# Performance work log

Measured on AMD Instinct MI355X. Metric: run time of the kernel, lower is better.

Reference implementation:

```python
import jax, jax.numpy as jnp
import numpy as np

B, S, D, H, N = 2, 2048, 768, 12, 128  # batch, seq_len, d_model, n_heads, num_segments
EPS_LN = 1e-5


def _layer_norm(x, g, b):
    m = x.mean(-1, keepdims=True)
    v = ((x - m) ** 2).mean(-1, keepdims=True)
    return (x - m) / jnp.sqrt(v + EPS_LN) * g + b


def _mha(q, k, v, Wqkv, bqkv, Wo, bo, n_heads):
    """torch.nn.MultiheadAttention (batch_first), returns (out, head-averaged attn)."""
    d = q.shape[-1]
    dh = d // n_heads
    Wq, Wk, Wv = jnp.split(Wqkv, 3, axis=0)
    bq, bk, bv = jnp.split(bqkv, 3)
    qh = (q @ Wq.T + bq).reshape(q.shape[0], q.shape[1], n_heads, dh)
    kh = (k @ Wk.T + bk).reshape(k.shape[0], k.shape[1], n_heads, dh)
    vh = (v @ Wv.T + bv).reshape(v.shape[0], v.shape[1], n_heads, dh)
    scores = jnp.einsum('bqhd,bkhd->bhqk', qh, kh) / jnp.sqrt(jnp.asarray(dh, q.dtype))
    attn = jax.nn.softmax(scores, axis=-1)                      # [B,H,Sq,Sk]
    out = jnp.einsum('bhqk,bkhd->bqhd', attn, vh).reshape(q.shape[0], q.shape[1], d)
    return out @ Wo.T + bo, attn.mean(axis=1)                   # attn avg over heads


def _aggregate(x, w, seg):  # per-batch: weighted mean of tokens into N segments
    num = jax.ops.segment_sum(w[:, None] * x, seg, num_segments=N)
    den = jax.ops.segment_sum(w, seg, num_segments=N)
    return num / (den[:, None] + 1e-8)


def setup_inputs() -> dict:
    key = jax.random.key(0)
    ks = jax.random.split(key, 16)
    s = 0.02
    inp = {
        'hidden_states': jax.random.normal(ks[0], (B, S, D), jnp.float32),
        'token_to_segment': jnp.sort(jax.random.randint(ks[1], (B, S), 0, N), axis=-1),
        # token_attention (shared for node-level self-attn in the adjacency=None branch)
        'Wqkv_t': jax.random.normal(ks[2], (3 * D, D), jnp.float32) * s,
        'bqkv_t': jnp.zeros((3 * D,), jnp.float32),
        'Wo_t': jax.random.normal(ks[3], (D, D), jnp.float32) * s,
        'bo_t': jnp.zeros((D,), jnp.float32),
        # cross_attention
        'Wqkv_c': jax.random.normal(ks[4], (3 * D, D), jnp.float32) * s,
        'bqkv_c': jnp.zeros((3 * D,), jnp.float32),
        'Wo_c': jax.random.normal(ks[5], (D, D), jnp.float32) * s,
        'bo_c': jnp.zeros((D,), jnp.float32),
        # layer norms
        'g_tok': jnp.ones((D,), jnp.float32),
        'b_tok': jnp.zeros((D,), jnp.float32),
        'g_node': jnp.ones((D,), jnp.float32),
        'b_node': jnp.zeros((D,), jnp.float32),
        # output projection
        'W_out': jax.random.normal(ks[6], (D, D), jnp.float32) * s,
        'b_out': jnp.zeros((D,), jnp.float32),
    }
    return inp


def reference(hidden_states, token_to_segment, Wqkv_t, bqkv_t, Wo_t, bo_t,
              Wqkv_c, bqkv_c, Wo_c, bo_c, g_tok, b_tok, g_node, b_node,
              W_out, b_out):
    hs = hidden_states
    # token-level self-attention + residual norm
    tok_attn_out, tok_attn = _mha(hs, hs, hs, Wqkv_t, bqkv_t, Wo_t, bo_t, H)
    token_output = _layer_norm(hs + tok_attn_out, g_tok, b_tok)
    # token -> node attention-weighted scatter aggregation
    w = tok_attn.mean(axis=1)  # [B,S] attention received per token
    node_emb = jax.vmap(_aggregate)(token_output, w, token_to_segment)  # [B,N,D]
    # node-level self-attention (reuses token_attention weights; adjacency=None path)
    node_out, node_attn = _mha(node_emb, node_emb, node_emb, Wqkv_t, bqkv_t, Wo_t, bo_t, H)
    node_emb = _layer_norm(node_emb + node_out, g_node, b_node)
    # cross-attention: tokens attend to nodes
    cross_out, cross_w = _mha(token_output, node_emb, node_emb, Wqkv_c, bqkv_c, Wo_c, bo_c, H)
    token_output = token_output + cross_out
    # node -> token gather + additive combine
    gathered = jnp.take_along_axis(node_emb, token_to_segment[:, :, None], axis=1)  # [B,S,D]
    enhanced = token_output + gathered
    output = enhanced @ W_out.T + b_out
    return output, node_emb, tok_attn, node_attn, cross_w
```

## Files before the change

### kernel.cpp

```cpp
#include <hip/hip_runtime.h>
#include <cstdint>

#define B_ 2
#define S_ 2048
#define D_ 768
#define H_ 12
#define DH_ 64
#define N_ 128

typedef unsigned short u16;
typedef unsigned int u32;
typedef unsigned long long u64;
typedef __attribute__((ext_vector_type(8))) short short8;
typedef __attribute__((ext_vector_type(4))) float f32x4;

#define MFMA16(a, b, c) __builtin_amdgcn_mfma_f32_16x16x32_bf16(a, b, c, 0, 0, 0)

__device__ inline u16 f2bf(float f) {
  union { float f; u32 u; } v; v.f = f;
  u32 r = v.u + 0x7FFFu + ((v.u >> 16) & 1u);
  return (u16)(r >> 16);
}
__device__ inline u32 pk2(float a, float b) {
  return (u32)f2bf(a) | ((u32)f2bf(b) << 16);
}
__device__ inline float bf2f(u16 h) {
  union { u32 u; float f; } v; v.u = ((u32)h) << 16;
  return v.f;
}
__device__ inline float wredmax(float v) {
  #pragma unroll
  for (int o = 32; o > 0; o >>= 1) v = fmaxf(v, __shfl_down(v, o));
  return v;
}
__device__ inline float wredsum(float v) {
  #pragma unroll
  for (int o = 32; o > 0; o >>= 1) v += __shfl_down(v, o);
  return v;
}
__device__ inline void async_lds16(const u16* g, u16* l) {
  __builtin_amdgcn_global_load_lds((const __attribute__((address_space(1))) void*)g,
                                   (__attribute__((address_space(3))) void*)l, 16, 0, 0);
}

__global__ void conv_bf16(const float* __restrict__ in, u16* __restrict__ outp, int n8) {
  int i = blockIdx.x * 256 + threadIdx.x;
  if (i >= n8) return;
  const float4* p = (const float4*)(in + (size_t)i * 8);
  float4 a = p[0], b = p[1];
  uint4 u;
  u.x = pk2(a.x, a.y); u.y = pk2(a.z, a.w); u.z = pk2(b.x, b.y); u.w = pk2(b.z, b.w);
  *(uint4*)(outp + (size_t)i * 8) = u;
}

template <int OUT_BF16>
__global__ __launch_bounds__(256) void gemm_bf16(
    const u16* __restrict__ A, int lda,
    const u16* __restrict__ W, int ldb,
    const float* __restrict__ bias,
    void* __restrict__ Cout, int ldc, int K) {
  __shared__ u16 As[128 * 32];
  __shared__ u16 Ws[128 * 32];
  const int tid = threadIdx.x;
  const int m0 = blockIdx.y * 128, n0 = blockIdx.x * 128;
  const int w = tid >> 6, lane = tid & 63;
  const int msub = (w & 1) * 64, nsub = (w >> 1) * 64;
  const int lrow = lane & 15, quad = lane >> 4;
  const int e0 = tid * 8;
  const int r0 = e0 >> 5, c0 = e0 & 31;
  const int e1 = e0 + 2048;
  const int r1 = e1 >> 5, c1 = e1 & 31;
  const u16* Ag0 = A + (size_t)(m0 + r0) * lda + c0;
  const u16* Ag1 = A + (size_t)(m0 + r1) * lda + c1;
  const u16* Wg0 = W + (size_t)(n0 + r0) * ldb + c0;
  const u16* Wg1 = W + (size_t)(n0 + r1) * ldb + c1;
  u16* AsB0 = As + (w << 9);
  u16* AsB1 = As + 2048 + (w << 9);
  u16* WsB0 = Ws + (w << 9);
  u16* WsB1 = Ws + 2048 + (w << 9);
  f32x4 zero = {0.f, 0.f, 0.f, 0.f};
  f32x4 acc[4][4];
  #pragma unroll
  for (int i = 0; i < 4; i++)
    #pragma unroll
    for (int j = 0; j < 4; j++) acc[i][j] = zero;
  for (int k0 = 0; k0 < K; k0 += 32) {
    __syncthreads();
    async_lds16(Ag0 + k0, AsB0);
    async_lds16(Ag1 + k0, AsB1);
    async_lds16(Wg0 + k0, WsB0);
    async_lds16(Wg1 + k0, WsB1);
    __syncthreads();
    short8 af[4], bf[4];
    #pragma unroll
    for (int i = 0; i < 4; i++)
      af[i] = *(const short8*)(As + (msub + i * 16 + lrow) * 32 + quad * 8);
    #pragma unroll
    for (int j = 0; j < 4; j++)
      bf[j] = *(const short8*)(Ws + (nsub + j * 16 + lrow) * 32 + quad * 8);
    #pragma unroll
    for (int i = 0; i < 4; i++)
      #pragma unroll
      for (int j = 0; j < 4; j++)
        acc[i][j] = MFMA16(af[i], bf[j], acc[i][j]);
  }
  #pragma unroll
  for (int i = 0; i < 4; i++) {
    #pragma unroll
    for (int j = 0; j < 4; j++) {
      int col = n0 + nsub + j * 16 + lrow;
      float bv = bias ? bias[col] : 0.f;
      #pragma unroll
      for (int r = 0; r < 4; r++) {
        int row = m0 + msub + i * 16 + quad * 4 + r;
        float val = acc[i][j][r] + bv;
        if (OUT_BF16) ((u16*)Cout)[(size_t)row * ldc + col] = f2bf(val);
        else ((float*)Cout)[(size_t)row * ldc + col] = val;
      }
    }
  }
}

__global__ __launch_bounds__(256) void transpose_v(const u16* __restrict__ qkv, u16* __restrict__ VT) {
  __shared__ u16 t[64][72];
  const int z = blockIdx.y, b = z / 12, h = z - b * 12;
  const int s0 = blockIdx.x * 64;
  const int tid = threadIdx.x;
  {
    int r = tid >> 2, dp = (tid & 3) * 16;
    const u16* src = qkv + (size_t)b * 2048 * 2304 + (size_t)(s0 + r) * 2304 + 1536 + h * 64 + dp;
    *(uint4*)&t[r][dp] = *(const uint4*)src;
    *(uint4*)&t[r][dp + 8] = *(const uint4*)(src + 8);
  }
  __syncthreads();
  int d = tid >> 2, sp = (tid & 3) * 16;
  u16 vals[16];
  #pragma unroll
  for (int i = 0; i < 16; i++) vals[i] = t[sp + i][d];
  u16* dst = VT + ((size_t)z * 64 + d) * 2048 + s0 + sp;
  *(uint4*)dst = *(uint4*)&vals[0];
  *(uint4*)(dst + 8) = *(uint4*)&vals[8];
}

__global__ __launch_bounds__(512, 2) void fused_tok_attn(
    const u16* __restrict__ qkv, const u16* __restrict__ VT,
    float* __restrict__ am, u16* __restrict__ attnout) {
  __shared__ u16 pbuf[8][16][264];
  __shared__ float lred[8][16];
  __shared__ float obuf[8][16][66];
  const int tid = threadIdx.x;
  const int w = tid >> 6, lane = tid & 63;
  const int lrow = lane & 15, quad = lane >> 4;
  const int blk = blockIdx.x;
  const int b = blk >> 7, q0 = (blk & 127) << 4;
  const u16* qp = qkv + (size_t)b * 2048 * 2304;
  const u16* kp = qp + 768;
  const int strip = w * 256;
  float* amrow = am + (size_t)b * 2048 * 2048 + (size_t)(q0 + lrow) * 2048 + strip;
  u16* ob = attnout + (size_t)b * 2048 * 768 + (size_t)q0 * 768;
  u16* pb = &pbuf[w][0][0];
  const float c12 = 1.f / 12.f;
  f32x4 zero = {0.f, 0.f, 0.f, 0.f};
  float amreg[8][8];
  #pragma unroll
  for (int c = 0; c < 8; c++)
    #pragma unroll
    for (int e = 0; e < 8; e++) amreg[c][e] = 0.f;
  for (int h = 0; h < 12; h++) {
    const u16* qh = qp + (size_t)(q0 + lrow) * 2304 + h * 64 + quad * 8;
    short8 qf0 = *(const short8*)qh;
    short8 qf1 = *(const short8*)(qh + 32);
    float lsum = 0.f;
    #pragma unroll
    for (int t = 0; t < 16; t++) {
      const u16* kh = kp + (size_t)(strip + t * 16 + lrow) * 2304 + h * 64 + quad * 8;
      short8 kf0 = *(const short8*)kh;
      short8 kf1 = *(const short8*)(kh + 32);
      f32x4 sv = zero;
      sv = MFMA16(kf0, qf0, sv);
      sv = MFMA16(kf1, qf1, sv);
      float pe0 = __expf(sv[0] * 0.125f);
      float pe1 = __expf(sv[1] * 0.125f);
      float pe2 = __expf(sv[2] * 0.125f);
      float pe3 = __expf(sv[3] * 0.125f);
      lsum += (pe0 + pe1) + (pe2 + pe3);
      u32 w0 = pk2(pe0, pe1), w1 = pk2(pe2, pe3);
      *(u64*)(pb + lrow * 264 + t * 16 + quad * 4) = (u64)w0 | ((u64)w1 << 32);
    }
    lsum += __shfl_xor(lsum, 16);
    lsum += __shfl_xor(lsum, 32);
    if (lane < 16) lred[w][lane] = lsum;
    __syncthreads();
    float invq;
    float inv4[4];
    {
      float s = 0.f;
      #pragma unroll
      for (int w2 = 0; w2 < 8; w2++) s += lred[w2][lrow];
      invq = 1.f / s;
      #pragma unroll
      for (int r = 0; r < 4; r++) {
        float sr = 0.f;
        #pragma unroll
        for (int w2 = 0; w2 < 8; w2++) sr += lred[w2][quad * 4 + r];
        inv4[r] = 1.f / sr;
      }
    }
    f32x4 oacc[4];
    #pragma unroll
    for (int j = 0; j < 4; j++) oacc[j] = zero;
    const u16* vtp = VT + (size_t)(b * 12 + h) * 64 * 2048;
    #pragma unroll
    for (int c = 0; c < 8; c++) {
      short8 pf = *(const short8*)(pb + lrow * 264 + c * 32 + quad * 8);
      short8 vf[4];
      #pragma unroll
      for (int j = 0; j < 4; j++)
        vf[j] = *(const short8*)(vtp + (size_t)(j * 16 + lrow) * 2048 + strip + c * 32 + quad * 8);
      #pragma unroll
      for (int j = 0; j < 4; j++) oacc[j] = MFMA16(pf, vf[j], oacc[j]);
      #pragma unroll
      for (int e = 0; e < 8; e++)
        amreg[c][e] += bf2f((u16)pf[e]) * invq;
    }
    asm volatile("s_waitcnt lgkmcnt(0)" ::: "memory");
    __builtin_amdgcn_sched_barrier(0);
    #pragma unroll
    for (int j = 0; j < 4; j++)
      #pragma unroll
      for (int r = 0; r < 4; r++)
        obuf[w][quad * 4 + r][j * 16 + lrow] = oacc[j][r] * inv4[r];
    __syncthreads();
    #pragma unroll
    for (int ee = 0; ee < 2; ee++) {
      int e2 = tid + ee * 512;
      int row = e2 >> 6, col = e2 & 63;
      float s = 0.f;
      #pragma unroll
      for (int w2 = 0; w2 < 8; w2++) s += obuf[w2][row][col];
      ob[(size_t)row * 768 + h * 64 + col] = f2bf(s);
    }
    __syncthreads();
  }
  #pragma unroll
  for (int c = 0; c < 8; c++) {
    float4 v0 = {amreg[c][0] * c12, amreg[c][1] * c12, amreg[c][2] * c12, amreg[c][3] * c12};
    float4 v1 = {amreg[c][4] * c12, amreg[c][5] * c12, amreg[c][6] * c12, amreg[c][7] * c12};
    *(float4*)(amrow + c * 32 + quad * 8) = v0;
    *(float4*)(amrow + c * 32 + quad * 8 + 4) = v1;
  }
}

__global__ __launch_bounds__(256) void qk_mfma(
    const u16* __restrict__ Q, int ldq, long qbs,
    const u16* __restrict__ Kp, int ldk, long kbs,
    float* __restrict__ S, long szs, int Sk, int nh, float scale) {
  __shared__ u16 Qs[128 * 72];
  __shared__ u16 Ks[128 * 72];
  const int tid = threadIdx.x;
  const int z = blockIdx.z, bb = z / nh, h = z - bb * nh;
  const u16* qp = Q + (size_t)bb * qbs + h * 64;
  const u16* kp = Kp + (size_t)bb * kbs + h * 64;
  float* sp = S + (size_t)z * szs;
  const int m0 = blockIdx.y * 128, n0 = blockIdx.x * 128;
  const int w = tid >> 6, lane = tid & 63;
  const int msub = (w & 1) * 64, nsub = (w >> 1) * 64;
  const int lrow = lane & 15, quad = lane >> 4;
  const int srow = tid >> 1, shalf = tid & 1;
  {
    const uint4* qg = (const uint4*)(qp + (size_t)(m0 + srow) * ldq + shalf * 32);
    const uint4* kg = (const uint4*)(kp + (size_t)(n0 + srow) * ldk + shalf * 32);
    uint4* qd = (uint4*)(Qs + srow * 72 + shalf * 32);
    uint4* kd = (uint4*)(Ks + srow * 72 + shalf * 32);
    #pragma unroll
    for (int u = 0; u < 4; u++) { qd[u] = qg[u]; kd[u] = kg[u]; }
  }
  __syncthreads();
  f32x4 zero = {0.f, 0.f, 0.f, 0.f};
  f32x4 acc[4][4];
  #pragma unroll
  for (int i = 0; i < 4; i++)
    #pragma unroll
    for (int j = 0; j < 4; j++) acc[i][j] = zero;
  #pragma unroll
  for (int ks = 0; ks < 2; ks++) {
    short8 af[4], bf[4];
    #pragma unroll
    for (int i = 0; i < 4; i++)
      af[i] = *(const short8*)(Qs + (msub + i * 16 + lrow) * 72 + ks * 32 + quad * 8);
    #pragma unroll
    for (int j = 0; j < 4; j++)
      bf[j] = *(const short8*)(Ks + (nsub + j * 16 + lrow) * 72 + ks * 32 + quad * 8);
    #pragma unroll
    for (int i = 0; i < 4; i++)
      #pragma unroll
      for (int j = 0; j < 4; j++)
        acc[i][j] = MFMA16(af[i], bf[j], acc[i][j]);
  }
  #pragma unroll
  for (int i = 0; i < 4; i++)
    #pragma unroll
    for (int j = 0; j < 4; j++) {
      int col = n0 + nsub + j * 16 + lrow;
      #pragma unroll
      for (int r = 0; r < 4; r++) {
        int row = m0 + msub + i * 16 + quad * 4 + r;
        sp[(size_t)row * Sk + col] = acc[i][j][r] * scale;
      }
    }
}

__global__ __launch_bounds__(128) void softmax_small(
    float* __restrict__ Sc, float* __restrict__ wout, int Sq) {
  const int q = blockIdx.x, b = blockIdx.y, tid = threadIdx.x;
  const int w = tid >> 6, lane = tid & 63;
  __shared__ float red[2];
  float am = 0.f;
  const size_t plane = (size_t)Sq * 128;
  for (int h = 0; h < 12; h++) {
    const int z = b * 12 + h;
    float* row = Sc + (size_t)z * plane + (size_t)q * 128;
    float v = row[tid];
    float m = wredmax(v);
    if (lane == 0) red[w] = m;
    __syncthreads();
    m = fmaxf(red[0], red[1]);
    float e = __expf(v - m);
    float s = wredsum(e);
    __syncthreads();
    if (lane == 0) red[w] = s;
    __syncthreads();
    float p = e / (red[0] + red[1]);
    ((u16*)(Sc + (size_t)z * plane))[(size_t)q * 256 + tid] = f2bf(p);
    am += p;
    __syncthreads();
  }
  wout[((size_t)b * Sq + q) * 128 + tid] = am * (1.f / 12.f);
}

__global__ __launch_bounds__(256) void pv_small(
    const u16* __restrict__ Pb, long pzs,
    const u16* __restrict__ KVb, int ldv, long vbs, int vhoff,
    u16* __restrict__ Outb, long obs) {
  __shared__ u16 Ps[128 * 40];
  __shared__ u16 Vs[64 * 40];
  const int tid = threadIdx.x;
  const int z = blockIdx.y, b = z / 12, h = z - b * 12;
  const u16* Pp = Pb + (size_t)z * pzs;
  const u16* Vp = KVb + (size_t)b * vbs + vhoff + h * 64;
  u16* Op = Outb + (size_t)b * obs + h * 64;
  const int m0 = blockIdx.x * 128;
  const int w = tid >> 6, lane = tid & 63;
  const int msub = w * 32;
  const int lrow = lane & 15, quad = lane >> 4;
  const int srow = tid >> 1, shalf = tid & 1;
  const int vk = tid >> 3, vn = (tid & 7) * 8;
  f32x4 zero = {0.f, 0.f, 0.f, 0.f};
  f32x4 acc[2][4];
  #pragma unroll
  for (int i = 0; i < 2; i++)
    #pragma unroll
    for (int j = 0; j < 4; j++) acc[i][j] = zero;
  #pragma unroll
  for (int k0 = 0; k0 < 128; k0 += 32) {
    uint4 pa = *(const uint4*)(Pp + (size_t)(m0 + srow) * 256 + k0 + shalf * 16);
    uint4 pb2 = *(const uint4*)(Pp + (size_t)(m0 + srow) * 256 + k0 + shalf * 16 + 8);
    uint4 vv = *(const uint4*)(Vp + (size_t)(k0 + vk) * ldv + vn);
    __syncthreads();
    *(uint4*)(Ps + srow * 40 + shalf * 16) = pa;
    *(uint4*)(Ps + srow * 40 + shalf * 16 + 8) = pb2;
    const u16* vs = (const u16*)&vv;
    #pragma unroll
    for (int u = 0; u < 8; u++) Vs[(vn + u) * 40 + vk] = vs[u];
    __syncthreads();
    short8 af[2], bf[4];
    #pragma unroll
    for (int i = 0; i < 2; i++)
      af[i] = *(const short8*)(Ps + (msub + i * 16 + lrow) * 40 + quad * 8);
    #pragma unroll
    for (int j = 0; j < 4; j++)
      bf[j] = *(const short8*)(Vs + (j * 16 + lrow) * 40 + quad * 8);
    #pragma unroll
    for (int i = 0; i < 2; i++)
      #pragma unroll
      for (int j = 0; j < 4; j++)
        acc[i][j] = MFMA16(af[i], bf[j], acc[i][j]);
  }
  #pragma unroll
  for (int i = 0; i < 2; i++)
    #pragma unroll
    for (int j = 0; j < 4; j++) {
      int col = j * 16 + lrow;
      #pragma unroll
      for (int r = 0; r < 4; r++) {
        int row = m0 + msub + i * 16 + quad * 4 + r;
        Op[(size_t)row * D_ + col] = f2bf(acc[i][j][r]);
      }
    }
}

__global__ void ln_kernel(const float* __restrict__ x1, const float* __restrict__ x2,
                          const float* __restrict__ g, const float* __restrict__ bt,
                          float* __restrict__ outp, u16* __restrict__ outbf) {
  const int row = blockIdx.x;
  const int tid = threadIdx.x;
  __shared__ float red[8];
  float v[3];
  #pragma unroll
  for (int j = 0; j < 3; j++) {
    int c = tid + j * 256;
    v[j] = x1[(size_t)row * D_ + c] + x2[(size_t)row * D_ + c];
  }
  float s = v[0] + v[1] + v[2];
  s = wredsum(s);
  int wid = tid >> 6, lane = tid & 63;
  if (lane == 0) red[wid] = s;
  __syncthreads();
  float mean = (red[0] + red[1] + red[2] + red[3]) / 768.f;
  float d0 = v[0] - mean, d1 = v[1] - mean, d2 = v[2] - mean;
  float q = d0 * d0 + d1 * d1 + d2 * d2;
  q = wredsum(q);
  if (lane == 0) red[4 + wid] = q;
  __syncthreads();
  float var = (red[4] + red[5] + red[6] + red[7]) / 768.f;
  float inv = rsqrtf(var + 1e-5f);
  #pragma unroll
  for (int j = 0; j < 3; j++) {
    int c = tid + j * 256;
    float val = (v[j] - mean) * inv * g[c] + bt[c];
    outp[(size_t)row * D_ + c] = val;
    if (outbf) outbf[(size_t)row * D_ + c] = f2bf(val);
  }
}

__global__ void colmean_part(const float* __restrict__ ta, float* __restrict__ part) {
  int b = blockIdx.y, z = blockIdx.z;
  int k = blockIdx.x * 256 + threadIdx.x;
  const float* p = ta + (size_t)b * S_ * S_ + (size_t)z * 256 * S_ + k;
  float s = 0.f;
  #pragma unroll 8
  for (int q = 0; q < 256; q++) s += p[(size_t)q * S_];
  part[((size_t)z * B_ + b) * S_ + k] = s;
}

__global__ void colmean_final(const float* __restrict__ part, float* __restrict__ w) {
  int b = blockIdx.y;
  int k = blockIdx.x * 256 + threadIdx.x;
  float s = 0.f;
  #pragma unroll
  for (int z = 0; z < 8; z++) s += part[((size_t)z * B_ + b) * S_ + k];
  w[b * S_ + k] = s * (1.f / (float)S_);
}

__global__ void aggregate_kernel(const float* __restrict__ x, const float* __restrict__ w,
                                 const int* __restrict__ seg, float* __restrict__ outp,
                                 u16* __restrict__ outbf) {
  const int b = blockIdx.y, n = blockIdx.x;
  const int* sg = seg + b * S_;
  int l = 0, rr = S_;
  while (l < rr) { int mid = (l + rr) >> 1; if (sg[mid] < n) l = mid + 1; else rr = mid; }
  const int lo = l;
  rr = S_;
  while (l < rr) { int mid = (l + rr) >> 1; if (sg[mid] < n + 1) l = mid + 1; else rr = mid; }
  const int hi = l;
  const int tid = threadIdx.x;
  float acc[3] = {0.f, 0.f, 0.f};
  float den = 0.f;
  for (int s = lo; s < hi; s++) {
    float ww = w[b * S_ + s];
    den += ww;
    const float* xr = x + (size_t)(b * S_ + s) * D_;
    #pragma unroll
    for (int j = 0; j < 3; j++) acc[j] += ww * xr[tid + j * 256];
  }
  float invd = 1.f / (den + 1e-8f);
  size_t ro = (size_t)(b * N_ + n) * D_;
  #pragma unroll
  for (int j = 0; j < 3; j++) {
    float val = acc[j] * invd;
    outp[ro + tid + j * 256] = val;
    outbf[ro + tid + j * 256] = f2bf(val);
  }
}

__global__ void enhanced_kernel(const float* __restrict__ tokout, const float* __restrict__ crossp,
                                const float* __restrict__ nodeemb, const int* __restrict__ seg,
                                u16* __restrict__ outbf) {
  int g8 = blockIdx.x * 256 + threadIdx.x;
  int bs = g8 / 96, d0 = (g8 - bs * 96) * 8;
  int b = bs >> 11;
  int n = seg[bs];
  const float* t = tokout + (size_t)bs * D_ + d0;
  const float* cp = crossp + (size_t)bs * D_ + d0;
  const float* ne = nodeemb + (size_t)(b * N_ + n) * D_ + d0;
  float4 a0 = *(const float4*)t, a1 = *(const float4*)(t + 4);
  float4 b0 = *(const float4*)cp, b1 = *(const float4*)(cp + 4);
  float4 c0 = *(const float4*)ne, c1 = *(const float4*)(ne + 4);
  uint4 u;
  u.x = pk2(a0.x + b0.x + c0.x, a0.y + b0.y + c0.y);
  u.y = pk2(a0.z + b0.z + c0.z, a0.w + b0.w + c0.w);
  u.z = pk2(a1.x + b1.x + c1.x, a1.y + b1.y + c1.y);
  u.w = pk2(a1.z + b1.z + c1.z, a1.w + b1.w + c1.w);
  *(uint4*)(outbf + (size_t)g8 * 8) = u;
}

extern "C" void kernel_launch(void* const* d_in, const int* in_sizes, int n_in,
                              void* d_out, int out_size, void* d_ws, size_t ws_size,
                              hipStream_t stream) {
  const float* hs     = (const float*)d_in[0];
  const int*   t2s    = (const int*)d_in[1];
  const float* Wqkv_t = (const float*)d_in[2];
  const float* bqkv_t = (const float*)d_in[3];
  const float* Wo_t   = (const float*)d_in[4];
  const float* bo_t   = (const float*)d_in[5];
  const float* Wqkv_c = (const float*)d_in[6];
  const float* bqkv_c = (const float*)d_in[7];
  const float* Wo_c   = (const float*)d_in[8];
  const float* bo_c   = (const float*)d_in[9];
  const float* g_tok  = (const float*)d_in[10];
  const float* b_tok  = (const float*)d_in[11];
  const float* g_node = (const float*)d_in[12];
  const float* b_node = (const float*)d_in[13];
  const float* W_out  = (const float*)d_in[14];
  const float* b_out  = (const float*)d_in[15];

  float* ws = (float*)d_ws;
  u16*   qkvbf       = (u16*)ws;
  u16*   enh_bf      = (u16*)ws;
  u16*   crossqbf    = (u16*)(ws + 1572864);
  u16*   crossattn_bf= (u16*)(ws + 3145728);
  float* R1 = ws + 4718592;
  u16*   hs_bf   = (u16*)R1;
  u16*   wqkvt1  = (u16*)(R1 + 1572864);
  u16*   VT      = (u16*)R1;
  float* projbuf = R1;
  float* Snode   = R1;
  u16*   wqkvt2  = (u16*)(R1 + 4000000);
  u16*   wot     = (u16*)(R1 + 6291456);
  u16*   wqkvc   = (u16*)R1;
  u16*   woc     = (u16*)(R1 + 6291456);
  u16*   wout    = (u16*)(R1 + 6586368);
  float* Scross  = R1;
  float* crossproj = R1;
  float* R2 = ws + 13107200;
  u16*   attnout_bf = (u16*)R2;
  u16*   tokout_bf  = (u16*)R2;
  float* wvec       = R2 + 1572864;
  float* colpart    = R2 + 1576960;
  float* nodepre    = R2 + 1609728;
  float* nodeproj   = R2 + 1806336;
  u16*   nodepre_bf = (u16*)(R2 + 2002944);
  u16*   nodeattn_bf= (u16*)(R2 + 2101248);
  u16*   nodeemb_bf = (u16*)(R2 + 2199552);
  u16*   nodeqkvbf  = (u16*)(R2 + 2297856);
  u16*   crosskvbf  = (u16*)(R2 + 2592768);
  float* tokout = ws + 16252928;

  float* outp       = (float*)d_out;
  float* o_output   = outp;
  float* o_nodeemb  = outp + 3145728;
  float* o_tokattn  = o_nodeemb + 196608;
  float* o_nodeattn = o_tokattn + 8388608;
  float* o_crossw   = o_nodeattn + 32768;

  conv_bf16<<<1536, 256, 0, stream>>>(hs, hs_bf, 393216);
  conv_bf16<<<864, 256, 0, stream>>>(Wqkv_t, wqkvt1, 221184);
  gemm_bf16<1><<<dim3(18, 32), 256, 0, stream>>>(hs_bf, 768, wqkvt1, 768, bqkv_t, qkvbf, 2304, 768);

  transpose_v<<<dim3(32, 24), 256, 0, stream>>>(qkvbf, VT);
  fused_tok_attn<<<256, 512, 0, stream>>>(qkvbf, VT, o_tokattn, attnout_bf);

  conv_bf16<<<288, 256, 0, stream>>>(Wo_t, wot, 73728);
  gemm_bf16<0><<<dim3(6, 32), 256, 0, stream>>>(attnout_bf, 768, wot, 768, bo_t, projbuf, 768, 768);
  ln_kernel<<<4096, 256, 0, stream>>>(hs, projbuf, g_tok, b_tok, tokout, tokout_bf);

  colmean_part<<<dim3(8, 2, 8), 256, 0, stream>>>(o_tokattn, colpart);
  colmean_final<<<dim3(8, 2), 256, 0, stream>>>(colpart, wvec);
  aggregate_kernel<<<dim3(128, 2), 256, 0, stream>>>(tokout, wvec, t2s, nodepre, nodepre_bf);
  conv_bf16<<<864, 256, 0, stream>>>(Wqkv_t, wqkvt2, 221184);
  gemm_bf16<1><<<dim3(18, 2), 256, 0, stream>>>(nodepre_bf, 768, wqkvt2, 768, bqkv_t, nodeqkvbf, 2304, 768);
  qk_mfma<<<dim3(1, 1, 24), 256, 0, stream>>>(
      nodeqkvbf, 2304, (long)128 * 2304, nodeqkvbf + 768, 2304, (long)128 * 2304,
      Snode, 16384, 128, 12, 0.125f);
  softmax_small<<<dim3(128, 2), 128, 0, stream>>>(Snode, o_nodeattn, 128);
  pv_small<<<dim3(1, 24), 256, 0, stream>>>(
      (const u16*)Snode, 32768, nodeqkvbf, 2304, (long)128 * 2304, 1536,
      nodeattn_bf, (long)128 * 768);
  gemm_bf16<0><<<dim3(6, 2), 256, 0, stream>>>(nodeattn_bf, 768, wot, 768, bo_t, nodeproj, 768, 768);
  ln_kernel<<<256, 256, 0, stream>>>(nodepre, nodeproj, g_node, b_node, o_nodeemb, nodeemb_bf);

  conv_bf16<<<864, 256, 0, stream>>>(Wqkv_c, wqkvc, 221184);
  conv_bf16<<<288, 256, 0, stream>>>(Wo_c, woc, 73728);
  conv_bf16<<<288, 256, 0, stream>>>(W_out, wout, 73728);
  gemm_bf16<1><<<dim3(6, 32), 256, 0, stream>>>(tokout_bf, 768, wqkvc, 768, bqkv_c, crossqbf, 768, 768);
  gemm_bf16<1><<<dim3(12, 2), 256, 0, stream>>>(nodeemb_bf, 768, wqkvc + 768 * 768, 768, bqkv_c + 768,
                                                crosskvbf, 1536, 768);

  qk_mfma<<<dim3(1, 16, 24), 256, 0, stream>>>(
      crossqbf, 768, (long)2048 * 768, crosskvbf, 1536, (long)128 * 1536,
      Scross, 262144, 128, 12, 0.125f);
  softmax_small<<<dim3(2048, 2), 128, 0, stream>>>(Scross, o_crossw, 2048);
  pv_small<<<dim3(16, 24), 256, 0, stream>>>(
      (const u16*)Scross, 524288, crosskvbf, 1536, (long)128 * 1536, 768,
      crossattn_bf, (long)2048 * 768);

  gemm_bf16<0><<<dim3(6, 32), 256, 0, stream>>>(crossattn_bf, 768, woc, 768, bo_c, crossproj, 768, 768);
  enhanced_kernel<<<1536, 256, 0, stream>>>(tokout, crossproj, o_nodeemb, t2s, enh_bf);
  gemm_bf16<0><<<dim3(6, 32), 256, 0, stream>>>(enh_bf, 768, wout, 768, b_out, o_output, 768, 768);
}
```

Before: 626.1 us.

## Split token-attention heads across two blocks and add a head-mean combine pass

```diff
diff --git a/kernel.cpp b/kernel.cpp
--- a/kernel.cpp
+++ b/kernel.cpp
@@ -142,31 +142,31 @@
   *(uint4*)(dst + 8) = *(uint4*)&vals[8];
 }
 
-__global__ __launch_bounds__(512, 2) void fused_tok_attn(
+__global__ __launch_bounds__(512, 4) void fused_tok_attn(
     const u16* __restrict__ qkv, const u16* __restrict__ VT,
-    float* __restrict__ am, u16* __restrict__ attnout) {
+    float* __restrict__ amF, u16* __restrict__ amH, u16* __restrict__ attnout) {
   __shared__ u16 pbuf[8][16][264];
   __shared__ float lred[8][16];
-  __shared__ float obuf[8][16][66];
+  __shared__ float obuf[2][16][66];
   const int tid = threadIdx.x;
   const int w = tid >> 6, lane = tid & 63;
   const int lrow = lane & 15, quad = lane >> 4;
-  const int blk = blockIdx.x;
-  const int b = blk >> 7, q0 = (blk & 127) << 4;
+  const int b = blockIdx.y, q0 = blockIdx.x << 4, z = blockIdx.z;
+  const int h0 = z * 6;
   const u16* qp = qkv + (size_t)b * 2048 * 2304;
   const u16* kp = qp + 768;
   const int strip = w * 256;
-  float* amrow = am + (size_t)b * 2048 * 2048 + (size_t)(q0 + lrow) * 2048 + strip;
+  const int jj = w & 3, shalf = w >> 2;
   u16* ob = attnout + (size_t)b * 2048 * 768 + (size_t)q0 * 768;
   u16* pb = &pbuf[w][0][0];
-  const float c12 = 1.f / 12.f;
   f32x4 zero = {0.f, 0.f, 0.f, 0.f};
   float amreg[8][8];
   #pragma unroll
   for (int c = 0; c < 8; c++)
     #pragma unroll
     for (int e = 0; e < 8; e++) amreg[c][e] = 0.f;
-  for (int h = 0; h < 12; h++) {
+  for (int hh = 0; hh < 6; hh++) {
+    const int h = h0 + hh;
     const u16* qh = qp + (size_t)(q0 + lrow) * 2304 + h * 64 + quad * 8;
     short8 qf0 = *(const short8*)qh;
     short8 qf1 = *(const short8*)(qh + 32);
@@ -206,49 +206,77 @@
         inv4[r] = 1.f / sr;
       }
     }
-    f32x4 oacc[4];
-    #pragma unroll
-    for (int j = 0; j < 4; j++) oacc[j] = zero;
-    const u16* vtp = VT + (size_t)(b * 12 + h) * 64 * 2048;
     #pragma unroll
     for (int c = 0; c < 8; c++) {
       short8 pf = *(const short8*)(pb + lrow * 264 + c * 32 + quad * 8);
-      short8 vf[4];
-      #pragma unroll
-      for (int j = 0; j < 4; j++)
-        vf[j] = *(const short8*)(vtp + (size_t)(j * 16 + lrow) * 2048 + strip + c * 32 + quad * 8);
-      #pragma unroll
-      for (int j = 0; j < 4; j++) oacc[j] = MFMA16(pf, vf[j], oacc[j]);
       #pragma unroll
       for (int e = 0; e < 8; e++)
         amreg[c][e] += bf2f((u16)pf[e]) * invq;
     }
-    asm volatile("s_waitcnt lgkmcnt(0)" ::: "memory");
-    __builtin_amdgcn_sched_barrier(0);
-    #pragma unroll
-    for (int j = 0; j < 4; j++)
-      #pragma unroll
-      for (int r = 0; r < 4; r++)
-        obuf[w][quad * 4 + r][j * 16 + lrow] = oacc[j][r] * inv4[r];
+    f32x4 oacc = zero;
+    {
+      const u16* vtp = VT + (size_t)(b * 12 + h) * 64 * 2048;
+      const u16* vbase = vtp + (size_t)(jj * 16 + lrow) * 2048 + shalf * 1024 + quad * 8;
+      const u16* pbase = &pbuf[shalf * 4][lrow][quad * 8];
+      #pragma unroll
+      for (int cc = 0; cc < 32; cc++) {
+        short8 pf = *(const short8*)(pbase + (cc >> 3) * (16 * 264) + (cc & 7) * 32);
+        short8 vf = *(const short8*)(vbase + cc * 32);
+        oacc = MFMA16(pf, vf, oacc);
+      }
+    }
+    #pragma unroll
+    for (int r = 0; r < 4; r++)
+      obuf[shalf][quad * 4 + r][jj * 16 + lrow] = oacc[r] * inv4[r];
     __syncthreads();
     #pragma unroll
     for (int ee = 0; ee < 2; ee++) {
       int e2 = tid + ee * 512;
       int row = e2 >> 6, col = e2 & 63;
-      float s = 0.f;
-      #pragma unroll
-      for (int w2 = 0; w2 < 8; w2++) s += obuf[w2][row][col];
+      float s = obuf[0][row][col] + obuf[1][row][col];
       ob[(size_t)row * 768 + h * 64 + col] = f2bf(s);
     }
-    __syncthreads();
-  }
-  #pragma unroll
-  for (int c = 0; c < 8; c++) {
-    float4 v0 = {amreg[c][0] * c12, amreg[c][1] * c12, amreg[c][2] * c12, amreg[c][3] * c12};
-    float4 v1 = {amreg[c][4] * c12, amreg[c][5] * c12, amreg[c][6] * c12, amreg[c][7] * c12};
-    *(float4*)(amrow + c * 32 + quad * 8) = v0;
-    *(float4*)(amrow + c * 32 + quad * 8 + 4) = v1;
-  }
+  }
+  if (z == 0) {
+    float* ar = amF + ((size_t)b * 2048 + q0 + lrow) * 2048 + strip;
+    #pragma unroll
+    for (int c = 0; c < 8; c++) {
+      float4 v0 = {amreg[c][0], amreg[c][1], amreg[c][2], amreg[c][3]};
+      float4 v1 = {amreg[c][4], amreg[c][5], amreg[c][6], amreg[c][7]};
+      *(float4*)(ar + c * 32 + quad * 8) = v0;
+      *(float4*)(ar + c * 32 + quad * 8 + 4) = v1;
+    }
+  } else {
+    u16* ar = amH + ((size_t)b * 2048 + q0 + lrow) * 2048 + strip;
+    #pragma unroll
+    for (int c = 0; c < 8; c++) {
+      uint4 u;
+      u.x = pk2(amreg[c][0], amreg[c][1]);
+      u.y = pk2(amreg[c][2], amreg[c][3]);
+      u.z = pk2(amreg[c][4], amreg[c][5]);
+      u.w = pk2(amreg[c][6], amreg[c][7]);
+      *(uint4*)(ar + c * 32 + quad * 8) = u;
+    }
+  }
+}
+
+__global__ void combine_am(float* __restrict__ amF, const u16* __restrict__ amH) {
+  size_t i = ((size_t)blockIdx.x * 256 + threadIdx.x) * 8;
+  float4 a0 = *(float4*)(amF + i);
+  float4 a1 = *(float4*)(amF + i + 4);
+  uint4 hb = *(const uint4*)(amH + i);
+  const float c12 = 1.f / 12.f;
+  float4 r0, r1;
+  r0.x = (a0.x + bf2f((u16)(hb.x & 0xffff))) * c12;
+  r0.y = (a0.y + bf2f((u16)(hb.x >> 16))) * c12;
+  r0.z = (a0.z + bf2f((u16)(hb.y & 0xffff))) * c12;
+  r0.w = (a0.w + bf2f((u16)(hb.y >> 16))) * c12;
+  r1.x = (a1.x + bf2f((u16)(hb.z & 0xffff))) * c12;
+  r1.y = (a1.y + bf2f((u16)(hb.z >> 16))) * c12;
+  r1.z = (a1.z + bf2f((u16)(hb.w & 0xffff))) * c12;
+  r1.w = (a1.w + bf2f((u16)(hb.w >> 16))) * c12;
+  *(float4*)(amF + i) = r0;
+  *(float4*)(amF + i + 4) = r1;
 }
 
 __global__ __launch_bounds__(256) void qk_mfma(
@@ -533,6 +561,7 @@
   u16*   hs_bf   = (u16*)R1;
   u16*   wqkvt1  = (u16*)(R1 + 1572864);
   u16*   VT      = (u16*)R1;
+  u16*   amh     = (u16*)(R1 + 4194304);
   float* projbuf = R1;
   float* Snode   = R1;
   u16*   wqkvt2  = (u16*)(R1 + 4000000);
@@ -568,7 +597,8 @@
   gemm_bf16<1><<<dim3(18, 32), 256, 0, stream>>>(hs_bf, 768, wqkvt1, 768, bqkv_t, qkvbf, 2304, 768);
 
   transpose_v<<<dim3(32, 24), 256, 0, stream>>>(qkvbf, VT);
-  fused_tok_attn<<<256, 512, 0, stream>>>(qkvbf, VT, o_tokattn, attnout_bf);
+  fused_tok_attn<<<dim3(128, 2, 2), 512, 0, stream>>>(qkvbf, VT, o_tokattn, amh, attnout_bf);
+  combine_am<<<4096, 256, 0, stream>>>(o_tokattn, amh);
 
   conv_bf16<<<288, 256, 0, stream>>>(Wo_t, wot, 73728);
   gemm_bf16<0><<<dim3(6, 32), 256, 0, stream>>>(attnout_bf, 768, wot, 768, bo_t, projbuf, 768, 768);
```

Result: no change. 629.9 us (+0.6%).
